# Performance work log

Hardware: AMD Instinct MI355X
Metric: run time of the kernel (lower is better)

Reference implementation:

```python
import jax, jax.numpy as jnp
import numpy as np

N_NODES = 50000
N_EDGES = 800000
D = 256
VOCAB = 50000
N_ETYPES = 3
N_STEPS = 5
N_GRAPHS = 64


def setup_inputs() -> dict:
    key = jax.random.key(0)
    ks = jax.random.split(key, 16)
    s = 1.0 / np.sqrt(D)
    return {
        "x": jax.random.randint(ks[0], (N_NODES,), 0, VOCAB),
        "src": jax.random.randint(ks[1], (N_EDGES,), 0, N_NODES),
        "dst": jax.random.randint(ks[2], (N_EDGES,), 0, N_NODES),
        "etypes": jax.random.randint(ks[3], (N_EDGES,), 0, N_ETYPES),
        "seg_ids": jnp.sort(jax.random.randint(ks[4], (N_NODES,), 0, N_GRAPHS)),
        "num_graphs": N_GRAPHS,
        "emb": jax.random.normal(ks[5], (VOCAB, D), jnp.float32),
        "W_msg": jax.random.normal(ks[6], (N_ETYPES, D, D), jnp.float32) * s,
        "b_msg": jax.random.normal(ks[7], (N_ETYPES, D), jnp.float32) * s,
        "w_ih": jax.random.normal(ks[8], (3 * D, D), jnp.float32) * s,
        "w_hh": jax.random.normal(ks[9], (3 * D, D), jnp.float32) * s,
        "b_ih": jax.random.normal(ks[10], (3 * D,), jnp.float32) * s,
        "b_hh": jax.random.normal(ks[11], (3 * D,), jnp.float32) * s,
        "gate_w": jax.random.normal(ks[12], (D, 1), jnp.float32) * s,
        "gate_b": jax.random.normal(ks[13], (1,), jnp.float32) * s,
    }


def _gru_cell(a, h, w_ih, w_hh, b_ih, b_hh):
    # a, h: [N, D]; gates: [N, 3D]
    gi = a @ w_ih.T + b_ih
    gh = h @ w_hh.T + b_hh
    i_r, i_z, i_n = jnp.split(gi, 3, axis=-1)
    h_r, h_z, h_n = jnp.split(gh, 3, axis=-1)
    r = jax.nn.sigmoid(i_r + h_r)
    z = jax.nn.sigmoid(i_z + h_z)
    n = jnp.tanh(i_n + r * h_n)
    return (1.0 - z) * n + z * h


def reference(x, src, dst, etypes, seg_ids, num_graphs, emb, W_msg, b_msg,
              w_ih, w_hh, b_ih, b_hh, gate_w, gate_b):
    # Embedding lookup (dropout is identity in eval mode)
    h = emb[x]  # [N, D]

    # GatedGraphConv: n_steps of per-etype linear message + scatter-add + GRU
    for _ in range(N_STEPS):
        # per-node transform under every etype's weight: [n_etypes, N, D]
        t = jnp.einsum("nd,edf->enf", h, W_msg)
        msg = t[etypes, src] + b_msg[etypes]        # [E, D]
        a = jax.ops.segment_sum(msg, dst, num_segments=N_NODES)  # [N, D]
        h = _gru_cell(a, h, w_ih, w_hh, b_ih, b_hh)

    # GlobalAttentionPooling: gate score + segment softmax + weighted sum
    gate = (h @ gate_w + gate_b)[:, 0]  # [N]
    gmax = jax.ops.segment_max(gate, seg_ids, num_segments=num_graphs)
    e = jnp.exp(gate - gmax[seg_ids])
    denom = jax.ops.segment_sum(e, seg_ids, num_segments=num_graphs)
    alpha = e / denom[seg_ids]  # [N]
    out = jax.ops.segment_sum(h * alpha[:, None], seg_ids, num_segments=num_graphs)
    return out  # [num_graphs, D]
```

## Files before the change

kernel.cpp:

```cpp
#include <hip/hip_runtime.h>
#include <hip/hip_bf16.h>
#include <stdint.h>

#define N_NODESC 50000
#define NPAD     50048
#define N_EDGESC 800000
#define DIM      256
#define DIM3     768
#define NSTEPS   5
#define NGRAPH   64

typedef __attribute__((ext_vector_type(4))) float  f32x4;
typedef __attribute__((ext_vector_type(8))) short  short8;
typedef __attribute__((ext_vector_type(4))) unsigned short u16x4;
typedef __attribute__((ext_vector_type(4))) _Float16 f16x4;

__device__ float          g_hf[(size_t)NPAD * DIM];
__device__ unsigned short g_hb[(size_t)NPAD * DIM];
__device__ unsigned short g_p [(size_t)NPAD * DIM3];
__device__ unsigned short g_a [(size_t)NPAD * DIM];
__device__ _Float16       g_gi[(size_t)NPAD * DIM3];
__device__ _Float16       g_gh[(size_t)NPAD * DIM3];
__device__ unsigned short g_Wc[DIM * DIM3];
__device__ unsigned short g_WI[DIM3 * DIM];
__device__ unsigned short g_WH[DIM3 * DIM];
__device__ int            g_cnt[NPAD * 4];
__device__ int            g_rowoff[N_NODESC + 1];
__device__ int            g_cur[N_NODESC];
__device__ unsigned       g_eidx[N_EDGESC];
__device__ int            g_bsum[256];
__device__ int            g_boff[256];
__device__ float          g_gate[N_NODESC];
__device__ int            g_soff[NGRAPH + 1];
__device__ float          g_gmax[NGRAPH];
__device__ float          g_gden[NGRAPH];

__device__ __forceinline__ float bf2f(unsigned short u) {
  unsigned x = ((unsigned)u) << 16;
  return __builtin_bit_cast(float, x);
}
__device__ __forceinline__ unsigned short f2bf(float f) {
  unsigned u = __builtin_bit_cast(unsigned, f);
  u += 0x7fffu + ((u >> 16) & 1u);
  return (unsigned short)(u >> 16);
}
__device__ __forceinline__ float sigm(float x) { return 1.0f / (1.0f + expf(-x)); }

__device__ __forceinline__ void async16(const void* g, void* l) {
  __builtin_amdgcn_global_load_lds(
      (const __attribute__((address_space(1))) unsigned int*)g,
      (__attribute__((address_space(3))) unsigned int*)l, 16, 0, 0);
}


__global__ void k_zero_cnt() {
  int i = blockIdx.x * 256 + threadIdx.x;
  g_cnt[i] = 0;
}

__global__ void k_prep_w(const float* __restrict__ Wmsg, const float* __restrict__ wih,
                         const float* __restrict__ whh) {
  int i = blockIdx.x * 256 + threadIdx.x;
  if (i < 196608) {
    int f = i / 768, j = i - f * 768;
    int e = j >> 8, d = j & 255;
    g_Wc[i] = f2bf(Wmsg[(e << 16) + (d << 8) + f]);
  } else if (i < 393216) {
    int t = i - 196608;
    g_WI[t] = f2bf(wih[t]);
  } else if (i < 589824) {
    int t = i - 393216;
    g_WH[t] = f2bf(whh[t]);
  }
}

__global__ void k_embed(const int* __restrict__ x, const float* __restrict__ emb) {
  int i = blockIdx.x * 256 + threadIdx.x;
  int n = i >> 6, t = i & 63;
  if (n >= N_NODESC) return;
  float4 v = *(const float4*)(emb + (size_t)x[n] * DIM + t * 4);
  *(float4*)(g_hf + (size_t)n * DIM + t * 4) = v;
  u16x4 b = {f2bf(v.x), f2bf(v.y), f2bf(v.z), f2bf(v.w)};
  *(u16x4*)(g_hb + (size_t)n * DIM + t * 4) = b;
}

__global__ void k_count(const int* __restrict__ dst, const int* __restrict__ et) {
  int e = blockIdx.x * 256 + threadIdx.x;
  if (e >= N_EDGESC) return;
  atomicAdd(&g_cnt[dst[e] * 4 + et[e]], 1);
}

__global__ void k_scan1() {
  __shared__ int lds[256];
  int n = blockIdx.x * 256 + threadIdx.x;
  int deg = (n < N_NODESC) ? (g_cnt[n * 4] + g_cnt[n * 4 + 1] + g_cnt[n * 4 + 2]) : 0;
  lds[threadIdx.x] = deg;
  __syncthreads();
  for (int o = 128; o > 0; o >>= 1) {
    if (threadIdx.x < o) lds[threadIdx.x] += lds[threadIdx.x + o];
    __syncthreads();
  }
  if (threadIdx.x == 0) g_bsum[blockIdx.x] = lds[0];
}

__global__ void k_scan2() {
  __shared__ int lds[256];
  int t = threadIdx.x;
  int v = (t < 196) ? g_bsum[t] : 0;
  lds[t] = v;
  __syncthreads();
  for (int o = 1; o < 256; o <<= 1) {
    int u = (t >= o) ? lds[t - o] : 0;
    __syncthreads();
    lds[t] += u;
    __syncthreads();
  }
  if (t < 196) g_boff[t] = lds[t] - v;
}

__global__ void k_scan3() {
  __shared__ int lds[256];
  int n = blockIdx.x * 256 + threadIdx.x;
  int t = threadIdx.x;
  int deg = (n < N_NODESC) ? (g_cnt[n * 4] + g_cnt[n * 4 + 1] + g_cnt[n * 4 + 2]) : 0;
  lds[t] = deg;
  __syncthreads();
  for (int o = 1; o < 256; o <<= 1) {
    int u = (t >= o) ? lds[t - o] : 0;
    __syncthreads();
    lds[t] += u;
    __syncthreads();
  }
  if (n < N_NODESC) {
    int off = g_boff[blockIdx.x] + lds[t] - deg;
    g_rowoff[n] = off;
    g_cur[n] = off;
  }
  if (n == N_NODESC - 1) g_rowoff[N_NODESC] = g_boff[blockIdx.x] + lds[t];
}

__global__ void k_fill(const int* __restrict__ src, const int* __restrict__ dst,
                       const int* __restrict__ et) {
  int e = blockIdx.x * 256 + threadIdx.x;
  if (e >= N_EDGESC) return;
  int p = atomicAdd(&g_cur[dst[e]], 1);
  g_eidx[p] = (((unsigned)src[e]) << 2) | (unsigned)et[e];
}

__global__ void k_segoff(const int* __restrict__ seg) {
  int n = blockIdx.x * 256 + threadIdx.x;
  if (n >= N_NODESC) return;
  int g = seg[n];
  int gp = (n == 0) ? -1 : seg[n - 1];
  for (int t = gp + 1; t <= g; ++t) g_soff[t] = n;
  if (n == N_NODESC - 1)
    for (int t = g + 1; t <= NGRAPH; ++t) g_soff[t] = N_NODESC;
}


#define ACC_ET(hv, et)                                                        \
  {                                                                           \
    float x0 = bf2f(hv[0]), x1 = bf2f(hv[1]), x2 = bf2f(hv[2]), x3 = bf2f(hv[3]); \
    if (et == 0)      { a0[0] += x0; a0[1] += x1; a0[2] += x2; a0[3] += x3; } \
    else if (et == 1) { a1[0] += x0; a1[1] += x1; a1[2] += x2; a1[3] += x3; } \
    else              { a2[0] += x0; a2[1] += x1; a2[2] += x2; a2[3] += x3; } \
  }

__global__ __launch_bounds__(256) void k_agg() {
  int node = blockIdx.x * 4 + (threadIdx.x >> 6);
  int lane = threadIdx.x & 63;
  if (node >= N_NODESC) return;
  float a0[4] = {0.f, 0.f, 0.f, 0.f};
  float a1[4] = {0.f, 0.f, 0.f, 0.f};
  float a2[4] = {0.f, 0.f, 0.f, 0.f};
  int s = g_rowoff[node], e = g_rowoff[node + 1];
  int i = s;
  for (; i + 4 <= e; i += 4) {
    unsigned v0 = g_eidx[i], v1 = g_eidx[i + 1], v2 = g_eidx[i + 2], v3 = g_eidx[i + 3];
    u16x4 hv0 = *(const u16x4*)(g_hb + (size_t)(v0 >> 2) * DIM + lane * 4);
    u16x4 hv1 = *(const u16x4*)(g_hb + (size_t)(v1 >> 2) * DIM + lane * 4);
    u16x4 hv2 = *(const u16x4*)(g_hb + (size_t)(v2 >> 2) * DIM + lane * 4);
    u16x4 hv3 = *(const u16x4*)(g_hb + (size_t)(v3 >> 2) * DIM + lane * 4);
    int e0 = (int)(v0 & 3u), e1 = (int)(v1 & 3u), e2 = (int)(v2 & 3u), e3 = (int)(v3 & 3u);
    ACC_ET(hv0, e0);
    ACC_ET(hv1, e1);
    ACC_ET(hv2, e2);
    ACC_ET(hv3, e3);
  }
  for (; i < e; ++i) {
    unsigned v = g_eidx[i];
    u16x4 hv = *(const u16x4*)(g_hb + (size_t)(v >> 2) * DIM + lane * 4);
    int et = (int)(v & 3u);
    ACC_ET(hv, et);
  }
  size_t base = (size_t)node * DIM3 + lane * 4;
  u16x4 o0 = {f2bf(a0[0]), f2bf(a0[1]), f2bf(a0[2]), f2bf(a0[3])};
  u16x4 o1 = {f2bf(a1[0]), f2bf(a1[1]), f2bf(a1[2]), f2bf(a1[3])};
  u16x4 o2 = {f2bf(a2[0]), f2bf(a2[1]), f2bf(a2[2]), f2bf(a2[3])};
  *(u16x4*)(g_p + base)       = o0;
  *(u16x4*)(g_p + base + 256) = o1;
  *(u16x4*)(g_p + base + 512) = o2;
}

template <int MODE>
__global__ __launch_bounds__(256) void k_gemm(const float* __restrict__ bias,
                                              const float* __restrict__ bmsg) {
  constexpr int K  = (MODE == 0) ? DIM3 : DIM;
  constexpr int NC = (MODE == 0) ? DIM : DIM3;
  const unsigned short* __restrict__ A  = (MODE == 0) ? g_p  : (MODE == 1) ? g_a  : g_hb;
  const unsigned short* __restrict__ BT = (MODE == 0) ? g_Wc : (MODE == 1) ? g_WI : g_WH;

  __shared__ unsigned short lA[128 * 32];
  __shared__ unsigned short lB[128 * 32];
  const int tx = threadIdx.x;
  const int lane = tx & 63;
  const int wave = tx >> 6;
  const int wr = wave >> 1, wc = wave & 1;
  const int tileN = blockIdx.x * 128;
  const int tileM = blockIdx.y * 128;

  f32x4 acc[4][4];
#pragma unroll
  for (int m = 0; m < 4; ++m)
#pragma unroll
    for (int n = 0; n < 4; ++n) {
      acc[m][n][0] = 0.f; acc[m][n][1] = 0.f; acc[m][n][2] = 0.f; acc[m][n][3] = 0.f;
    }

  const int r0 = tx >> 2;
  const int c0 = (tx & 3) * 8;

  for (int k0 = 0; k0 < K; k0 += 32) {
#pragma unroll
    for (int i = 0; i < 2; ++i) {
      int row = i * 64 + r0;
      async16((const void*)(A + (size_t)(tileM + row) * K + k0 + c0),
              (void*)(lA + row * 32 + c0));
    }
#pragma unroll
    for (int i = 0; i < 2; ++i) {
      int row = i * 64 + r0;
      async16((const void*)(BT + (size_t)(tileN + row) * K + k0 + c0),
              (void*)(lB + row * 32 + c0));
    }
    __syncthreads();
    short8 af[4], bfr[4];
#pragma unroll
    for (int m = 0; m < 4; ++m)
      af[m] = *(const short8*)(lA + (wr * 64 + m * 16 + (lane & 15)) * 32 + (lane >> 4) * 8);
#pragma unroll
    for (int n = 0; n < 4; ++n)
      bfr[n] = *(const short8*)(lB + (wc * 64 + n * 16 + (lane & 15)) * 32 + (lane >> 4) * 8);
#pragma unroll
    for (int m = 0; m < 4; ++m)
#pragma unroll
      for (int n = 0; n < 4; ++n)
        acc[m][n] = __builtin_amdgcn_mfma_f32_16x16x32_bf16(af[m], bfr[n], acc[m][n], 0, 0, 0);
    __syncthreads();
  }

#pragma unroll
  for (int m = 0; m < 4; ++m) {
    int row0 = tileM + wr * 64 + m * 16 + (lane >> 4) * 4;
#pragma unroll
    for (int n = 0; n < 4; ++n) {
      int col = tileN + wc * 64 + n * 16 + (lane & 15);
      f32x4 v = acc[m][n];
#pragma unroll
      for (int r = 0; r < 4; ++r) {
        int row = row0 + r;
        float val = v[r];
        if (MODE == 0) {
          const int* c = g_cnt + (size_t)row * 4;
          val += c[0] * bmsg[col] + c[1] * bmsg[256 + col] + c[2] * bmsg[512 + col];
          g_a[(size_t)row * NC + col] = f2bf(val);
        } else if (MODE == 1) {
          val += bias[col];
          g_gi[(size_t)row * NC + col] = (_Float16)val;
        } else {
          val += bias[col];
          g_gh[(size_t)row * NC + col] = (_Float16)val;
        }
      }
    }
  }
}

template <int LAST>
__global__ void k_gru(const float* __restrict__ gw, const float* __restrict__ gb) {
  int i = blockIdx.x * 256 + threadIdx.x;
  int n = i >> 6, t = (i & 63) * 4;
  if (n >= N_NODESC) return;
  size_t b3 = (size_t)n * DIM3 + t;
  size_t b1 = (size_t)n * DIM + t;
  f16x4 ir4 = *(const f16x4*)(g_gi + b3);
  f16x4 iz4 = *(const f16x4*)(g_gi + b3 + 256);
  f16x4 in4 = *(const f16x4*)(g_gi + b3 + 512);
  f16x4 hr4 = *(const f16x4*)(g_gh + b3);
  f16x4 hz4 = *(const f16x4*)(g_gh + b3 + 256);
  f16x4 hn4 = *(const f16x4*)(g_gh + b3 + 512);
  float4 h = *(const float4*)(g_hf + b1);
  float4 o;
#pragma unroll
  for (int j = 0; j < 4; ++j) {
    float r = sigm((float)ir4[j] + (float)hr4[j]);
    float z = sigm((float)iz4[j] + (float)hz4[j]);
    float nn = tanhf((float)in4[j] + r * (float)hn4[j]);
    float hj = (j == 0) ? h.x : (j == 1) ? h.y : (j == 2) ? h.z : h.w;
    float oj = (1.f - z) * nn + z * hj;
    if (j == 0) o.x = oj; else if (j == 1) o.y = oj; else if (j == 2) o.z = oj; else o.w = oj;
  }
  *(float4*)(g_hf + b1) = o;
  u16x4 ob = {f2bf(o.x), f2bf(o.y), f2bf(o.z), f2bf(o.w)};
  *(u16x4*)(g_hb + b1) = ob;
  if (LAST) {
    float4 w = *(const float4*)(gw + t);
    float p = o.x * w.x + o.y * w.y + o.z * w.z + o.w * w.w;
    for (int off = 32; off > 0; off >>= 1) p += __shfl_xor(p, off);
    if ((threadIdx.x & 63) == 0) g_gate[n] = p + gb[0];
  }
}


__global__ void k_segred() {
  int g = blockIdx.x, t = threadIdx.x;
  __shared__ float red[256];
  int s = g_soff[g], e = g_soff[g + 1];
  float m = -3.4e38f;
  for (int n = s + t; n < e; n += 256) m = fmaxf(m, g_gate[n]);
  red[t] = m;
  __syncthreads();
  for (int o = 128; o > 0; o >>= 1) {
    if (t < o) red[t] = fmaxf(red[t], red[t + o]);
    __syncthreads();
  }
  m = red[0];
  __syncthreads();
  float sm = 0.f;
  for (int n = s + t; n < e; n += 256) sm += expf(g_gate[n] - m);
  red[t] = sm;
  __syncthreads();
  for (int o = 128; o > 0; o >>= 1) {
    if (t < o) red[t] += red[t + o];
    __syncthreads();
  }
  if (t == 0) {
    g_gmax[g] = m;
    g_gden[g] = (e > s && red[0] != 0.f) ? red[0] : 1.f;
  }
}

__global__ void k_zero_out(float* __restrict__ out) {
  out[blockIdx.x * 256 + threadIdx.x] = 0.f;
}

__global__ __launch_bounds__(256) void k_poolacc(const int* __restrict__ seg,
                                                 float* __restrict__ out) {
  __shared__ int   segL[128];
  __shared__ float alphaL[128];
  int base = blockIdx.x * 128;
  int t = threadIdx.x;
  if (t < 128) {
    int n = base + t;
    if (n < N_NODESC) {
      int g = seg[n];
      segL[t] = g;
      alphaL[t] = expf(g_gate[n] - g_gmax[g]) / g_gden[g];
    } else {
      segL[t] = -1;
    }
  }
  __syncthreads();
  float acc = 0.f;
  int gcur = segL[0];
  for (int j = 0; j < 128; ++j) {
    int gs = segL[j];
    if (gs < 0) break;
    if (gs != gcur) {
      atomicAdd(out + (size_t)gcur * DIM + t, acc);
      acc = 0.f;
      gcur = gs;
    }
    acc += alphaL[j] * g_hf[(size_t)(base + j) * DIM + t];
  }
  if (gcur >= 0) atomicAdd(out + (size_t)gcur * DIM + t, acc);
}


extern "C" void kernel_launch(void* const* d_in, const int* in_sizes, int n_in,
                              void* d_out, int out_size, void* d_ws, size_t ws_size,
                              hipStream_t stream) {
  const int* x = (const int*)d_in[0];
  const int* src = (const int*)d_in[1];
  const int* dst = (const int*)d_in[2];
  const int* ety = (const int*)d_in[3];
  const int* seg = (const int*)d_in[4];
  const float* emb = (const float*)d_in[6];
  const float* Wmsg = (const float*)d_in[7];
  const float* bmsg = (const float*)d_in[8];
  const float* wih = (const float*)d_in[9];
  const float* whh = (const float*)d_in[10];
  const float* bih = (const float*)d_in[11];
  const float* bhh = (const float*)d_in[12];
  const float* gw = (const float*)d_in[13];
  const float* gb = (const float*)d_in[14];
  float* out = (float*)d_out;

  k_zero_cnt<<<NPAD * 4 / 256, 256, 0, stream>>>();
  k_prep_w<<<2304, 256, 0, stream>>>(Wmsg, wih, whh);
  k_embed<<<12500, 256, 0, stream>>>(x, emb);
  k_count<<<(N_EDGESC + 255) / 256, 256, 0, stream>>>(dst, ety);
  k_scan1<<<196, 256, 0, stream>>>();
  k_scan2<<<1, 256, 0, stream>>>();
  k_scan3<<<196, 256, 0, stream>>>();
  k_fill<<<(N_EDGESC + 255) / 256, 256, 0, stream>>>(src, dst, ety);
  k_segoff<<<196, 256, 0, stream>>>(seg);

  for (int s = 0; s < NSTEPS; ++s) {
    k_agg<<<12500, 256, 0, stream>>>();
    k_gemm<0><<<dim3(2, 391), 256, 0, stream>>>(nullptr, bmsg);
    k_gemm<1><<<dim3(6, 391), 256, 0, stream>>>(bih, nullptr);
    k_gemm<2><<<dim3(6, 391), 256, 0, stream>>>(bhh, nullptr);
    if (s < NSTEPS - 1)
      k_gru<0><<<12500, 256, 0, stream>>>(nullptr, nullptr);
    else
      k_gru<1><<<12500, 256, 0, stream>>>(gw, gb);
  }

  k_segred<<<NGRAPH, 256, 0, stream>>>();
  k_zero_out<<<NGRAPH, 256, 0, stream>>>(out);
  k_poolacc<<<391, 256, 0, stream>>>(seg, out);
}
```

Before: 1.668 ms.

## Fuse GRU input/hidden GEMMs with GRU gate epilogue into one kernel

Replaces the two separate GRU GEMMs (which wrote fp16 gi/gh buffers of 3D per node) and the elementwise GRU kernel with a single kernel. It loads a 64-row tile of a and h into swizzled LDS, computes r/z/n gate pre-activations by MFMA with the input and hidden products summed for r and z, then applies the GRU update in registers. The weights are permuted at prep time so each wave's 16-column slab holds matching r, z, n columns. This removes the large gi/gh round trip through global memory, at the cost of B operands read straight from global/L2 without LDS reuse and a grid of only 782 blocks. The gate score is moved to a separate small kernel after the last step.

```diff
diff --git a/kernel.cpp b/kernel.cpp
--- a/kernel.cpp
+++ b/kernel.cpp
@@ -13,14 +13,11 @@
 typedef __attribute__((ext_vector_type(4))) float  f32x4;
 typedef __attribute__((ext_vector_type(8))) short  short8;
 typedef __attribute__((ext_vector_type(4))) unsigned short u16x4;
-typedef __attribute__((ext_vector_type(4))) _Float16 f16x4;
 
 __device__ float          g_hf[(size_t)NPAD * DIM];
 __device__ unsigned short g_hb[(size_t)NPAD * DIM];
 __device__ unsigned short g_p [(size_t)NPAD * DIM3];
 __device__ unsigned short g_a [(size_t)NPAD * DIM];
-__device__ _Float16       g_gi[(size_t)NPAD * DIM3];
-__device__ _Float16       g_gh[(size_t)NPAD * DIM3];
 __device__ unsigned short g_Wc[DIM * DIM3];
 __device__ unsigned short g_WI[DIM3 * DIM];
 __device__ unsigned short g_WH[DIM3 * DIM];
@@ -67,10 +64,14 @@
     g_Wc[i] = f2bf(Wmsg[(e << 16) + (d << 8) + f]);
   } else if (i < 393216) {
     int t = i - 196608;
-    g_WI[t] = f2bf(wih[t]);
+    int c = t >> 8, k = t & 255;
+    int j = c / 48, rem = c - j * 48, g = rem >> 4, f = rem & 15;
+    g_WI[t] = f2bf(wih[(g * 256 + j * 16 + f) * 256 + k]);
   } else if (i < 589824) {
     int t = i - 393216;
-    g_WH[t] = f2bf(whh[t]);
+    int c = t >> 8, k = t & 255;
+    int j = c / 48, rem = c - j * 48, g = rem >> 4, f = rem & 15;
+    g_WH[t] = f2bf(whh[(g * 256 + j * 16 + f) * 256 + k]);
   }
 }
 
@@ -202,13 +203,11 @@
   *(u16x4*)(g_p + base + 512) = o2;
 }
 
-template <int MODE>
-__global__ __launch_bounds__(256) void k_gemm(const float* __restrict__ bias,
-                                              const float* __restrict__ bmsg) {
-  constexpr int K  = (MODE == 0) ? DIM3 : DIM;
-  constexpr int NC = (MODE == 0) ? DIM : DIM3;
-  const unsigned short* __restrict__ A  = (MODE == 0) ? g_p  : (MODE == 1) ? g_a  : g_hb;
-  const unsigned short* __restrict__ BT = (MODE == 0) ? g_Wc : (MODE == 1) ? g_WI : g_WH;
+__global__ __launch_bounds__(256) void k_gemm0(const float* __restrict__ bmsg) {
+  constexpr int K = DIM3;
+  constexpr int NC = DIM;
+  const unsigned short* __restrict__ A  = g_p;
+  const unsigned short* __restrict__ BT = g_Wc;
 
   __shared__ unsigned short lA[128 * 32];
   __shared__ unsigned short lB[128 * 32];
@@ -269,58 +268,111 @@
 #pragma unroll
       for (int r = 0; r < 4; ++r) {
         int row = row0 + r;
-        float val = v[r];
-        if (MODE == 0) {
-          const int* c = g_cnt + (size_t)row * 4;
-          val += c[0] * bmsg[col] + c[1] * bmsg[256 + col] + c[2] * bmsg[512 + col];
-          g_a[(size_t)row * NC + col] = f2bf(val);
-        } else if (MODE == 1) {
-          val += bias[col];
-          g_gi[(size_t)row * NC + col] = (_Float16)val;
-        } else {
-          val += bias[col];
-          g_gh[(size_t)row * NC + col] = (_Float16)val;
-        }
+        const int* c = g_cnt + (size_t)row * 4;
+        float val = v[r] + c[0] * bmsg[col] + c[1] * bmsg[256 + col] + c[2] * bmsg[512 + col];
+        g_a[(size_t)row * NC + col] = f2bf(val);
       }
     }
   }
 }
 
-template <int LAST>
-__global__ void k_gru(const float* __restrict__ gw, const float* __restrict__ gb) {
-  int i = blockIdx.x * 256 + threadIdx.x;
-  int n = i >> 6, t = (i & 63) * 4;
-  if (n >= N_NODESC) return;
-  size_t b3 = (size_t)n * DIM3 + t;
-  size_t b1 = (size_t)n * DIM + t;
-  f16x4 ir4 = *(const f16x4*)(g_gi + b3);
-  f16x4 iz4 = *(const f16x4*)(g_gi + b3 + 256);
-  f16x4 in4 = *(const f16x4*)(g_gi + b3 + 512);
-  f16x4 hr4 = *(const f16x4*)(g_gh + b3);
-  f16x4 hz4 = *(const f16x4*)(g_gh + b3 + 256);
-  f16x4 hn4 = *(const f16x4*)(g_gh + b3 + 512);
-  float4 h = *(const float4*)(g_hf + b1);
-  float4 o;
-#pragma unroll
-  for (int j = 0; j < 4; ++j) {
-    float r = sigm((float)ir4[j] + (float)hr4[j]);
-    float z = sigm((float)iz4[j] + (float)hz4[j]);
-    float nn = tanhf((float)in4[j] + r * (float)hn4[j]);
-    float hj = (j == 0) ? h.x : (j == 1) ? h.y : (j == 2) ? h.z : h.w;
-    float oj = (1.f - z) * nn + z * hj;
-    if (j == 0) o.x = oj; else if (j == 1) o.y = oj; else if (j == 2) o.z = oj; else o.w = oj;
-  }
-  *(float4*)(g_hf + b1) = o;
-  u16x4 ob = {f2bf(o.x), f2bf(o.y), f2bf(o.z), f2bf(o.w)};
-  *(u16x4*)(g_hb + b1) = ob;
-  if (LAST) {
-    float4 w = *(const float4*)(gw + t);
-    float p = o.x * w.x + o.y * w.y + o.z * w.z + o.w * w.w;
-    for (int off = 32; off > 0; off >>= 1) p += __shfl_xor(p, off);
-    if ((threadIdx.x & 63) == 0) g_gate[n] = p + gb[0];
-  }
-}
-
+__global__ __launch_bounds__(256) void k_fused(const float* __restrict__ bih,
+                                               const float* __restrict__ bhh) {
+  __shared__ unsigned short lAa[64 * 256];
+  __shared__ unsigned short lAh[64 * 256];
+  const int tx = threadIdx.x;
+  const int lane = tx & 63;
+  const int wave = tx >> 6;
+  const int tileM = blockIdx.x * 64;
+
+#pragma unroll
+  for (int it = 0; it < 8; ++it) {
+    int o = it * 4096 + tx * 16;
+    int row = o >> 9;
+    int s = (o >> 4) & 31;
+    int cg = s ^ (row & 7);
+    int gelem = (tileM + row) * 256 + cg * 8;
+    async16((const void*)(g_a + gelem), (void*)((char*)lAa + o));
+    async16((const void*)(g_hb + gelem), (void*)((char*)lAh + o));
+  }
+  __syncthreads();
+
+  const int f = lane & 15;
+  const int q = lane >> 4;
+  const int xr = f & 7;
+
+  for (int t = 0; t < 4; ++t) {
+    int j = wave + t * 4;
+    f32x4 acc[4][4];
+#pragma unroll
+    for (int m = 0; m < 4; ++m)
+#pragma unroll
+      for (int n = 0; n < 4; ++n) {
+        acc[m][n][0] = 0.f; acc[m][n][1] = 0.f; acc[m][n][2] = 0.f; acc[m][n][3] = 0.f;
+      }
+    const unsigned short* WIb = g_WI + (size_t)(48 * j + f) * 256;
+    const unsigned short* WHb = g_WH + (size_t)(48 * j + f) * 256;
+
+    for (int kk = 0; kk < 8; ++kk) {
+      short8 aa[4], ah[4];
+#pragma unroll
+      for (int m = 0; m < 4; ++m) {
+        int boff = (m * 16 + f) * 512 + (((kk * 4 + q) ^ xr) * 16);
+        aa[m] = *(const short8*)((const char*)lAa + boff);
+        ah[m] = *(const short8*)((const char*)lAh + boff);
+      }
+      int koff = kk * 32 + q * 8;
+      short8 bi0 = *(const short8*)(WIb + 0 * 4096 + koff);
+      short8 bi1 = *(const short8*)(WIb + 1 * 4096 + koff);
+      short8 bi2 = *(const short8*)(WIb + 2 * 4096 + koff);
+      short8 bh0 = *(const short8*)(WHb + 0 * 4096 + koff);
+      short8 bh1 = *(const short8*)(WHb + 1 * 4096 + koff);
+      short8 bh2 = *(const short8*)(WHb + 2 * 4096 + koff);
+#pragma unroll
+      for (int m = 0; m < 4; ++m) {
+        acc[m][0] = __builtin_amdgcn_mfma_f32_16x16x32_bf16(aa[m], bi0, acc[m][0], 0, 0, 0);
+        acc[m][0] = __builtin_amdgcn_mfma_f32_16x16x32_bf16(ah[m], bh0, acc[m][0], 0, 0, 0);
+        acc[m][1] = __builtin_amdgcn_mfma_f32_16x16x32_bf16(aa[m], bi1, acc[m][1], 0, 0, 0);
+        acc[m][1] = __builtin_amdgcn_mfma_f32_16x16x32_bf16(ah[m], bh1, acc[m][1], 0, 0, 0);
+        acc[m][2] = __builtin_amdgcn_mfma_f32_16x16x32_bf16(aa[m], bi2, acc[m][2], 0, 0, 0);
+        acc[m][3] = __builtin_amdgcn_mfma_f32_16x16x32_bf16(ah[m], bh2, acc[m][3], 0, 0, 0);
+      }
+    }
+
+    int d = j * 16 + f;
+    float biR = bih[d] + bhh[d];
+    float biZ = bih[256 + d] + bhh[256 + d];
+    float biN = bih[512 + d];
+    float bhN = bhh[512 + d];
+#pragma unroll
+    for (int m = 0; m < 4; ++m) {
+      int row0 = tileM + m * 16 + q * 4;
+#pragma unroll
+      for (int r = 0; r < 4; ++r) {
+        int row = row0 + r;
+        float rr = sigm(acc[m][0][r] + biR);
+        float zz = sigm(acc[m][1][r] + biZ);
+        float nn = tanhf(acc[m][2][r] + biN + rr * (acc[m][3][r] + bhN));
+        float ho = g_hf[(size_t)row * DIM + d];
+        float o = (1.f - zz) * nn + zz * ho;
+        g_hf[(size_t)row * DIM + d] = o;
+        g_hb[(size_t)row * DIM + d] = f2bf(o);
+      }
+    }
+  }
+}
+
+
+__global__ void k_gate(const float* __restrict__ gw, const float* __restrict__ gb) {
+  int node = blockIdx.x * 4 + (threadIdx.x >> 6);
+  int lane = threadIdx.x & 63;
+  if (node >= N_NODESC) return;
+  float4 h = *(const float4*)(g_hf + (size_t)node * DIM + lane * 4);
+  float4 w = *(const float4*)(gw + lane * 4);
+  float p = h.x * w.x + h.y * w.y + h.z * w.z + h.w * w.w;
+  for (int o = 32; o > 0; o >>= 1) p += __shfl_xor(p, o);
+  if (lane == 0) g_gate[node] = p + gb[0];
+}
 
 __global__ void k_segred() {
   int g = blockIdx.x, t = threadIdx.x;
@@ -418,15 +470,11 @@
 
   for (int s = 0; s < NSTEPS; ++s) {
     k_agg<<<12500, 256, 0, stream>>>();
-    k_gemm<0><<<dim3(2, 391), 256, 0, stream>>>(nullptr, bmsg);
-    k_gemm<1><<<dim3(6, 391), 256, 0, stream>>>(bih, nullptr);
-    k_gemm<2><<<dim3(6, 391), 256, 0, stream>>>(bhh, nullptr);
-    if (s < NSTEPS - 1)
-      k_gru<0><<<12500, 256, 0, stream>>>(nullptr, nullptr);
-    else
-      k_gru<1><<<12500, 256, 0, stream>>>(gw, gb);
-  }
-
+    k_gemm0<<<dim3(2, 391), 256, 0, stream>>>(bmsg);
+    k_fused<<<NPAD / 64, 256, 0, stream>>>(bih, bhh);
+  }
+
+  k_gate<<<12500, 256, 0, stream>>>(gw, gb);
   k_segred<<<NGRAPH, 256, 0, stream>>>();
   k_zero_out<<<NGRAPH, 256, 0, stream>>>(out);
   k_poolacc<<<391, 256, 0, stream>>>(seg, out);
```

Measured after the change: 2.267 ms. +35.9%, slower.
